# Performance work log

Measured on AMD Instinct MI355X. Metric: run time of the kernel, lower is better.

Reference implementation:

```python
import jax, jax.numpy as jnp
import numpy as np

LAMBDA = 0.7
RATIO = 3
EPS = 1e-6


def setup_inputs() -> dict:
    key = jax.random.key(0)
    k1, k2, k3 = jax.random.split(key, 3)
    bs, n, w, h = 8, 7, 640, 640
    preds = jax.random.normal(k1, (bs, n, w, h), dtype=jnp.float32)
    labels = jax.random.randint(k2, (bs, n, w, h), 0, 2, dtype=jnp.int32)
    training_mask = jax.random.randint(k3, (bs, w, h), 0, 2, dtype=jnp.int32)
    return {"preds": preds, "labels": labels, "training_mask": training_mask}


def _dice(S, G):
    # S, G: [C, P]; per-channel dice coefficient, then mean over channels
    num = 2.0 * jnp.sum(S * G, axis=-1)
    den = jnp.sum(S * S, axis=-1) + jnp.sum(G * G, axis=-1) + EPS
    return jnp.mean(num / den)


def _single_sample(pred, label, mask):
    # pred, label: [n, P]; mask: [P]
    P = pred.shape[-1]
    p = jax.nn.sigmoid(pred)
    pred_n = p[-1] * mask            # masked full-text prediction
    label_n = label[-1] * mask

    # --- OHEM mask M (cal_M): keep all positives + top (ratio*n_pos) hardest negatives ---
    pos = pred_n >= 0.5
    n_pos = jnp.sum(pos)
    n_neg_all = jnp.sum(~pos)
    k = n_pos * RATIO
    # sigmoid outputs are in (0,1); sentinel -1 pushes positives to the end of the descending sort
    neg_vals = jnp.where(pos, -1.0, pred_n)
    sorted_desc = -jnp.sort(-neg_vals)
    thr = sorted_desc[jnp.clip(k - 1, 0, P - 1)]  # k-th largest negative score
    ohem_active = (n_neg_all > k) & (k > 0)
    M = jnp.where(ohem_active, (pred_n >= thr).astype(jnp.float32), 1.0)

    # L_c: dice loss on OHEM-selected full-text map
    L_c = 1.0 - _dice((pred_n * M)[None, :], (label_n * M)[None, :])

    # L_s: dice loss on shrunk kernels, gated by predicted text region W
    W = (pred_n >= 0.5).astype(jnp.float32)
    L_s = 1.0 - _dice(p[:-1] * W, label[:-1] * W)

    loss = LAMBDA * L_c + (1.0 - LAMBDA) * L_s
    return L_c, L_s, loss


def reference(preds, labels, training_mask):
    bs, n, w, h = preds.shape
    preds = preds.reshape(bs, n, w * h)
    labels = labels.reshape(bs, n, w * h).astype(jnp.float32)
    mask = training_mask.reshape(bs, w * h).astype(jnp.float32)
    L_c, L_s, loss = jax.vmap(_single_sample)(preds, labels, mask)
    # reduction='mean'
    return L_c.mean(), L_s.mean(), loss.mean()
```

## Files before the change

kernel.cpp:

```cpp
#include <hip/hip_runtime.h>

#define BS   8
#define NCH  7
#define PX   409600
#define NBIN 65536
#define NCHK 256
#define EPSF 1e-6f
#define NT   256
#define GXM  50
#define UM   4
#define ITM  2

__device__ __forceinline__ float sigf(float x) {
    return 1.0f / (1.0f + __expf(-x));
}

__device__ __forceinline__ unsigned wred_u(unsigned v) {
    #pragma unroll
    for (int o = 32; o; o >>= 1) v += __shfl_down(v, o);
    return v;
}

__device__ __forceinline__ void wred3_f(float& v0, float& v1, float& v2) {
    #pragma unroll
    for (int o = 32; o; o >>= 1) {
        float t0 = __shfl_down(v0, o);
        float t1 = __shfl_down(v1, o);
        float t2 = __shfl_down(v2, o);
        v0 += t0; v1 += t1; v2 += t2;
    }
}

__device__ void select2(const unsigned* __restrict__ chunks,
                        const unsigned* __restrict__ bins,
                        unsigned k, unsigned* out_bin, unsigned* out_rank) {
    __shared__ unsigned cs[256];
    int t = threadIdx.x;
    cs[t] = chunks[t];
    __syncthreads();
    #pragma unroll
    for (int off = 1; off < 256; off <<= 1) {
        unsigned v = cs[t];
        unsigned a = (t + off < 256) ? cs[t + off] : 0u;
        __syncthreads();
        cs[t] = v + a;
        __syncthreads();
    }
    {
        unsigned sfx  = cs[t];
        unsigned sfx1 = (t < 255) ? cs[t + 1] : 0u;
        if (sfx >= k && sfx1 < k) { *out_bin = (unsigned)t; *out_rank = k - sfx1; }
    }
    __syncthreads();
    unsigned chunk = *out_bin, krem = *out_rank;
    cs[t] = bins[chunk * 256 + t];
    __syncthreads();
    #pragma unroll
    for (int off = 1; off < 256; off <<= 1) {
        unsigned v = cs[t];
        unsigned a = (t + off < 256) ? cs[t + off] : 0u;
        __syncthreads();
        cs[t] = v + a;
        __syncthreads();
    }
    {
        unsigned sfx  = cs[t];
        unsigned sfx1 = (t < 255) ? cs[t + 1] : 0u;
        if (sfx >= krem && sfx1 < krem) {
            *out_bin  = chunk * 256 + (unsigned)t;
            *out_rank = krem - sfx1;
        }
    }
    __syncthreads();
}

__global__ __launch_bounds__(256) void k_main(
        const float* __restrict__ preds, const int* __restrict__ labels,
        const int* __restrict__ mask,
        float* __restrict__ psumA,
        unsigned* __restrict__ ppos,
        unsigned* __restrict__ pzero,
        float* __restrict__ psumB,
        unsigned* __restrict__ done) {
    const int tid = threadIdx.x;
    const int y = blockIdx.y;
    const int b = y / 6, c = y % 6;
    const int cb = blockIdx.x;
    const bool c0 = (c == 0);
    if (y == 0 && cb == 0 && tid == 0) *done = 0u;

    const float* pc = preds + ((size_t)b * NCH + c) * PX;
    const int*   lc = labels + ((size_t)b * NCH + c) * PX;
    const float* p6 = preds + ((size_t)b * NCH + 6) * PX;
    const int*   l6 = labels + ((size_t)b * NCH + 6) * PX;
    const int*   mk = mask + (size_t)b * PX;

    float sn = 0.f, sp = 0.f;
    unsigned slc = 0;
    float a0 = 0.f, a1 = 0.f;
    unsigned a2c = 0, cnt = 0;

    for (int it = 0; it < ITM; ++it) {
        const int gbase = cb * (NT * UM * ITM) + it * (NT * UM) + tid;
        float4 P6[UM]; int4 M[UM]; float4 P[UM]; int4 L[UM]; int4 L6[UM];
        #pragma unroll
        for (int q = 0; q < UM; q++) {
            int px = (gbase + q * NT) * 4;
            P6[q] = *(const float4*)(p6 + px);
            M[q]  = *(const int4*)(mk + px);
        }
        #pragma unroll
        for (int q = 0; q < UM; q++) {
            int px = (gbase + q * NT) * 4;
            P[q] = *(const float4*)(pc + px);
            L[q] = *(const int4*)(lc + px);
        }
        if (c0) {
            #pragma unroll
            for (int q = 0; q < UM; q++) {
                int px = (gbase + q * NT) * 4;
                L6[q] = *(const int4*)(l6 + px);
            }
        }
        __builtin_amdgcn_sched_barrier(0);

        #pragma unroll
        for (int q = 0; q < UM; q++) {
            float mm[4]  = {(float)M[q].x, (float)M[q].y, (float)M[q].z, (float)M[q].w};
            float p6a[4] = {P6[q].x, P6[q].y, P6[q].z, P6[q].w};
            float pa[4]  = {P[q].x, P[q].y, P[q].z, P[q].w};
            int   la[4]  = {L[q].x, L[q].y, L[q].z, L[q].w};
            int   l6a[4] = {L6[q].x, L6[q].y, L6[q].z, L6[q].w};
            #pragma unroll
            for (int v = 0; v < 4; v++) {
                float pn = sigf(p6a[v]) * mm[v];
                bool W   = (pn >= 0.5f);
                float s  = sigf(pa[v]);
                bool lw  = W && (la[v] != 0);
                sn += lw ? s : 0.0f;
                sp += W ? s * s : 0.0f;
                slc += lw ? 1u : 0u;
                if (c0) {
                    cnt += W ? 1u : (__float_as_uint(pn) == 0u ? 0x10000u : 0u);
                    bool ln = (l6a[v] != 0) && (mm[v] != 0.0f);
                    a0 += ln ? pn : 0.0f;
                    a1 += pn * pn;
                    a2c += ln ? 1u : 0u;
                }
            }
        }
    }

    __shared__ float red[4][3];
    __shared__ float redA[4][3];
    __shared__ unsigned redC[4];
    const int lane = tid & 63, wid = tid >> 6;
    float v0 = sn, v1 = sp, v2 = (float)slc;
    wred3_f(v0, v1, v2);
    if (lane == 0) { red[wid][0] = v0; red[wid][1] = v1; red[wid][2] = v2; }
    if (c0) {
        float u0 = a0, u1 = a1, u2 = (float)a2c;
        wred3_f(u0, u1, u2);
        unsigned cr = wred_u(cnt);
        if (lane == 0) { redA[wid][0] = u0; redA[wid][1] = u1; redA[wid][2] = u2; redC[wid] = cr; }
    }
    __syncthreads();
    if (tid < 3) {
        float tot = red[0][tid] + red[1][tid] + red[2][tid] + red[3][tid];
        psumB[((size_t)y * 3 + tid) * GXM + cb] = tot;
    }
    if (c0) {
        if (tid < 3) {
            float tot = redA[0][tid] + redA[1][tid] + redA[2][tid] + redA[3][tid];
            psumA[((size_t)b * 3 + tid) * GXM + cb] = tot;
        }
        if (tid == 3) {
            unsigned ct = redC[0] + redC[1] + redC[2] + redC[3];
            ppos[b * GXM + cb]  = ct & 0xFFFFu;
            pzero[b * GXM + cb] = ct >> 16;
        }
    }
}

__global__ __launch_bounds__(256) void k_sel(
        const float* __restrict__ preds, const int* __restrict__ labels,
        const int* __restrict__ mask,
        const float* __restrict__ psumA, const float* __restrict__ psumB,
        const unsigned* __restrict__ ppos, const unsigned* __restrict__ pzero,
        unsigned* __restrict__ histws, unsigned* __restrict__ chunkws,
        float* __restrict__ lcls, unsigned* __restrict__ done,
        float* __restrict__ out) {
    const int tid = threadIdx.x;
    const int b = blockIdx.x;
    const int lane = tid & 63, wid = tid >> 6;

    __shared__ float S[21];
    __shared__ unsigned C[2];
    if (tid < 21) S[tid] = 0.f;
    if (tid < 2) C[tid] = 0u;
    __syncthreads();
    {
        unsigned pc = 0, zc = 0;
        for (int i = tid; i < GXM; i += NT) {
            pc += ppos[b * GXM + i];
            zc += pzero[b * GXM + i];
        }
        pc = wred_u(pc); zc = wred_u(zc);
        if (lane == 0) { atomicAdd(&C[0], pc); atomicAdd(&C[1], zc); }
    }
    for (int i = tid; i < 3 * GXM; i += NT)
        atomicAdd(&S[18 + i / GXM], psumA[(size_t)b * 3 * GXM + i]);
    for (int i = tid; i < 6 * 3 * GXM; i += NT) {
        int cch = i / (3 * GXM);
        int j   = (i / GXM) % 3;
        atomicAdd(&S[j * 6 + cch], psumB[(size_t)b * 6 * 3 * GXM + i]);
    }
    __syncthreads();
    const unsigned np = C[0], zc = C[1];

    const unsigned k = np * 3u;
    const bool active = ((unsigned)PX - np > k) && (k > 0u);
    const unsigned nzneg = (unsigned)PX - np - zc;

    float Lc_b;
    if (!active || k >= nzneg) {
        Lc_b = 1.0f - 2.0f * S[18] / (S[19] + S[20] + EPSF);
    } else {
        unsigned* h1 = histws + (size_t)b * NBIN;
        unsigned* c1 = chunkws + (size_t)b * NCHK;
        const float* pr6 = preds + ((size_t)b * NCH + 6) * PX;
        const int*   lb6 = labels + ((size_t)b * NCH + 6) * PX;
        const int*   mk  = mask + (size_t)b * PX;

        for (int j = tid; j < NBIN; j += NT) h1[j] = 0u;
        for (int j = tid; j < NCHK; j += NT) c1[j] = 0u;
        __syncthreads();
        for (int gg = tid; gg < PX; gg += NT) {
            float pnx = sigf(pr6[gg]) * (float)mk[gg];
            if (pnx < 0.5f) {
                unsigned bits = __float_as_uint(pnx);
                if (bits) {
                    atomicAdd(&h1[bits >> 16], 1u);
                    atomicAdd(&c1[bits >> 24], 1u);
                }
            }
        }
        __syncthreads();
        if (tid == 0) { atomicAdd(&h1[0], zc); atomicAdd(&c1[0], zc); }
        __syncthreads();

        __shared__ unsigned rb, rr, rb2, rr2;
        select2(c1, h1, k, &rb, &rr);
        float thrv;
        if (rb == 0u) {
            thrv = 0.0f;
        } else {
            unsigned hi = rb;
            for (int j = tid; j < NBIN; j += NT) h1[j] = 0u;
            for (int j = tid; j < NCHK; j += NT) c1[j] = 0u;
            __syncthreads();
            for (int gg = tid; gg < PX; gg += NT) {
                float pnx = sigf(pr6[gg]) * (float)mk[gg];
                if (pnx < 0.5f) {
                    unsigned bits = __float_as_uint(pnx);
                    if (bits && (bits >> 16) == hi) {
                        unsigned lo = bits & 0xFFFFu;
                        atomicAdd(&h1[lo], 1u);
                        atomicAdd(&c1[lo >> 8], 1u);
                    }
                }
            }
            __syncthreads();
            select2(c1, h1, rr, &rb2, &rr2);
            thrv = __uint_as_float((hi << 16) | rb2);
        }
        float a0 = 0.f, a1 = 0.f, a2 = 0.f;
        for (int gg = tid; gg < PX; gg += NT) {
            float m   = (float)mk[gg];
            float pnx = sigf(pr6[gg]) * m;
            if (pnx >= thrv) {
                float ln = (float)lb6[gg] * m;
                a0 += pnx * ln;
                a1 += pnx * pnx;
                a2 += ln;
            }
        }
        __shared__ float aR[4][3];
        wred3_f(a0, a1, a2);
        if (lane == 0) { aR[wid][0] = a0; aR[wid][1] = a1; aR[wid][2] = a2; }
        __syncthreads();
        float A0 = aR[0][0] + aR[1][0] + aR[2][0] + aR[3][0];
        float A1 = aR[0][1] + aR[1][1] + aR[2][1] + aR[3][1];
        float A2 = aR[0][2] + aR[1][2] + aR[2][2] + aR[3][2];
        Lc_b = 1.0f - 2.0f * A0 / (A1 + A2 + EPSF);
    }

    float ls_acc = 0.f;
    #pragma unroll
    for (int c = 0; c < 6; c++)
        ls_acc += (2.0f * S[c]) / (S[6 + c] + S[12 + c] + EPSF);
    float Ls_b = 1.0f - ls_acc * (1.0f / 6.0f);

    if (tid == 0) {
        lcls[b * 2]     = Lc_b;
        lcls[b * 2 + 1] = Ls_b;
    }

    __shared__ unsigned tick;
    if (tid == 0) {
        __threadfence();
        tick = atomicAdd(done, 1u);
    }
    __syncthreads();
    if (tick != (unsigned)(BS - 1)) return;
    __threadfence();

    float Lc = 0.f, Ls = 0.f;
    if (tid < BS) { Lc = lcls[tid * 2]; Ls = lcls[tid * 2 + 1]; }
    #pragma unroll
    for (int o = 4; o; o >>= 1) { Lc += __shfl_down(Lc, o); Ls += __shfl_down(Ls, o); }
    if (tid == 0) {
        float lc_m = Lc * (1.0f / (float)BS);
        float ls_m = Ls * (1.0f / (float)BS);
        out[0] = lc_m;
        out[1] = ls_m;
        out[2] = 0.7f * lc_m + 0.3f * ls_m;
    }
}

extern "C" void kernel_launch(void* const* d_in, const int* in_sizes, int n_in,
                              void* d_out, int out_size, void* d_ws, size_t ws_size,
                              hipStream_t stream) {
    const float* preds = (const float*)d_in[0];
    const int* labels  = (const int*)d_in[1];
    const int* mask    = (const int*)d_in[2];
    float* out = (float*)d_out;

    float*    psumA   = (float*)d_ws;
    unsigned* ppos    = (unsigned*)(psumA + (size_t)BS * 3 * GXM);
    unsigned* pzero   = ppos + BS * GXM;
    float*    psumB   = (float*)(pzero + BS * GXM);
    unsigned* done    = (unsigned*)(psumB + (size_t)BS * 18 * GXM);
    float*    lcls    = (float*)(done + 8);
    unsigned* histws  = (unsigned*)(lcls + BS * 2);
    unsigned* chunkws = histws + (size_t)BS * NBIN;

    hipLaunchKernelGGL(k_main, dim3(GXM, BS * 6), dim3(NT), 0, stream,
                       preds, labels, mask, psumA, ppos, pzero, psumB, done);

    hipLaunchKernelGGL(k_sel, dim3(BS), dim3(NT), 0, stream,
                       preds, labels, mask, psumA, psumB, ppos, pzero,
                       histws, chunkws, lcls, done, out);
}
```

Before: 216.5 us.

## Process three kernel channels per block to reuse channel-6 and mask loads

Each k_main block now handles three shrunk-kernel channels instead of one, loading the full-text prediction and mask once per pixel and reusing them for all three channels. The grid shrinks from 48 to 16 rows per column, and ITM is raised so each block still covers the same pixel range. This cuts redundant reads of channel 6 and the mask and their sigmoid recomputation. In exchange there are fewer blocks in flight (800 vs 2400), which may lower memory-level parallelism.

```diff
diff --git a/kernel.cpp b/kernel.cpp
--- a/kernel.cpp
+++ b/kernel.cpp
@@ -8,8 +8,7 @@
 #define EPSF 1e-6f
 #define NT   256
 #define GXM  50
-#define UM   4
-#define ITM  2
+#define ITM  8
 
 __device__ __forceinline__ float sigf(float x) {
     return 1.0f / (1.0f + __expf(-x));
@@ -84,97 +83,96 @@
         unsigned* __restrict__ done) {
     const int tid = threadIdx.x;
     const int y = blockIdx.y;
-    const int b = y / 6, c = y % 6;
+    const int b = y >> 1, half = y & 1;
+    const int cbase = half * 3;
     const int cb = blockIdx.x;
-    const bool c0 = (c == 0);
+    const bool h0 = (half == 0);
     if (y == 0 && cb == 0 && tid == 0) *done = 0u;
 
-    const float* pc = preds + ((size_t)b * NCH + c) * PX;
-    const int*   lc = labels + ((size_t)b * NCH + c) * PX;
-    const float* p6 = preds + ((size_t)b * NCH + 6) * PX;
-    const int*   l6 = labels + ((size_t)b * NCH + 6) * PX;
-    const int*   mk = mask + (size_t)b * PX;
-
-    float sn = 0.f, sp = 0.f;
-    unsigned slc = 0;
+    const float* p6  = preds + ((size_t)b * NCH + 6) * PX;
+    const int*   l6  = labels + ((size_t)b * NCH + 6) * PX;
+    const int*   mk  = mask + (size_t)b * PX;
+    const float* pc0 = preds + ((size_t)b * NCH + cbase) * PX;
+    const int*   lc0 = labels + ((size_t)b * NCH + cbase) * PX;
+
+    float sn[3] = {0.f, 0.f, 0.f}, sp[3] = {0.f, 0.f, 0.f};
+    unsigned sl[3] = {0u, 0u, 0u};
     float a0 = 0.f, a1 = 0.f;
     unsigned a2c = 0, cnt = 0;
 
     for (int it = 0; it < ITM; ++it) {
-        const int gbase = cb * (NT * UM * ITM) + it * (NT * UM) + tid;
-        float4 P6[UM]; int4 M[UM]; float4 P[UM]; int4 L[UM]; int4 L6[UM];
+        const int g  = cb * (NT * ITM) + it * NT + tid;
+        const int px = g * 4;
+        float4 P6 = *(const float4*)(p6 + px);
+        int4   M  = *(const int4*)(mk + px);
+        int4   L6 = make_int4(0, 0, 0, 0);
+        if (h0) L6 = *(const int4*)(l6 + px);
+        float4 P[3]; int4 L[3];
         #pragma unroll
-        for (int q = 0; q < UM; q++) {
-            int px = (gbase + q * NT) * 4;
-            P6[q] = *(const float4*)(p6 + px);
-            M[q]  = *(const int4*)(mk + px);
-        }
+        for (int c = 0; c < 3; c++) {
+            P[c] = *(const float4*)(pc0 + (size_t)c * PX + px);
+            L[c] = *(const int4*)(lc0 + (size_t)c * PX + px);
+        }
+        __builtin_amdgcn_sched_barrier(0);
+
+        float mm[4]  = {(float)M.x, (float)M.y, (float)M.z, (float)M.w};
+        float p6a[4] = {P6.x, P6.y, P6.z, P6.w};
+        int   l6a[4] = {L6.x, L6.y, L6.z, L6.w};
         #pragma unroll
-        for (int q = 0; q < UM; q++) {
-            int px = (gbase + q * NT) * 4;
-            P[q] = *(const float4*)(pc + px);
-            L[q] = *(const int4*)(lc + px);
-        }
-        if (c0) {
+        for (int v = 0; v < 4; v++) {
+            float pn = sigf(p6a[v]) * mm[v];
+            bool W   = (pn >= 0.5f);
+            if (h0) {
+                cnt += W ? 1u : (__float_as_uint(pn) == 0u ? 0x10000u : 0u);
+                bool ln = (l6a[v] != 0) && (mm[v] != 0.0f);
+                a0 += ln ? pn : 0.0f;
+                a1 += pn * pn;
+                a2c += ln ? 1u : 0u;
+            }
+            float pv[3] = {((const float*)&P[0])[v], ((const float*)&P[1])[v],
+                           ((const float*)&P[2])[v]};
+            int   lv[3] = {((const int*)&L[0])[v], ((const int*)&L[1])[v],
+                           ((const int*)&L[2])[v]};
             #pragma unroll
-            for (int q = 0; q < UM; q++) {
-                int px = (gbase + q * NT) * 4;
-                L6[q] = *(const int4*)(l6 + px);
-            }
-        }
-        __builtin_amdgcn_sched_barrier(0);
-
-        #pragma unroll
-        for (int q = 0; q < UM; q++) {
-            float mm[4]  = {(float)M[q].x, (float)M[q].y, (float)M[q].z, (float)M[q].w};
-            float p6a[4] = {P6[q].x, P6[q].y, P6[q].z, P6[q].w};
-            float pa[4]  = {P[q].x, P[q].y, P[q].z, P[q].w};
-            int   la[4]  = {L[q].x, L[q].y, L[q].z, L[q].w};
-            int   l6a[4] = {L6[q].x, L6[q].y, L6[q].z, L6[q].w};
-            #pragma unroll
-            for (int v = 0; v < 4; v++) {
-                float pn = sigf(p6a[v]) * mm[v];
-                bool W   = (pn >= 0.5f);
-                float s  = sigf(pa[v]);
-                bool lw  = W && (la[v] != 0);
-                sn += lw ? s : 0.0f;
-                sp += W ? s * s : 0.0f;
-                slc += lw ? 1u : 0u;
-                if (c0) {
-                    cnt += W ? 1u : (__float_as_uint(pn) == 0u ? 0x10000u : 0u);
-                    bool ln = (l6a[v] != 0) && (mm[v] != 0.0f);
-                    a0 += ln ? pn : 0.0f;
-                    a1 += pn * pn;
-                    a2c += ln ? 1u : 0u;
-                }
-            }
-        }
-    }
-
-    __shared__ float red[4][3];
+            for (int c = 0; c < 3; c++) {
+                float s = sigf(pv[c]);
+                bool lw = W && (lv[c] != 0);
+                sn[c] += lw ? s : 0.0f;
+                sp[c] += W ? s * s : 0.0f;
+                sl[c] += lw ? 1u : 0u;
+            }
+        }
+    }
+
+    __shared__ float red[4][3][3];
     __shared__ float redA[4][3];
     __shared__ unsigned redC[4];
     const int lane = tid & 63, wid = tid >> 6;
-    float v0 = sn, v1 = sp, v2 = (float)slc;
-    wred3_f(v0, v1, v2);
-    if (lane == 0) { red[wid][0] = v0; red[wid][1] = v1; red[wid][2] = v2; }
-    if (c0) {
+    #pragma unroll
+    for (int c = 0; c < 3; c++) {
+        float v0 = sn[c], v1 = sp[c], v2 = (float)sl[c];
+        wred3_f(v0, v1, v2);
+        if (lane == 0) { red[wid][c][0] = v0; red[wid][c][1] = v1; red[wid][c][2] = v2; }
+    }
+    if (h0) {
         float u0 = a0, u1 = a1, u2 = (float)a2c;
         wred3_f(u0, u1, u2);
         unsigned cr = wred_u(cnt);
         if (lane == 0) { redA[wid][0] = u0; redA[wid][1] = u1; redA[wid][2] = u2; redC[wid] = cr; }
     }
     __syncthreads();
-    if (tid < 3) {
-        float tot = red[0][tid] + red[1][tid] + red[2][tid] + red[3][tid];
-        psumB[((size_t)y * 3 + tid) * GXM + cb] = tot;
-    }
-    if (c0) {
-        if (tid < 3) {
-            float tot = redA[0][tid] + redA[1][tid] + redA[2][tid] + redA[3][tid];
-            psumA[((size_t)b * 3 + tid) * GXM + cb] = tot;
-        }
-        if (tid == 3) {
+    if (tid < 9) {
+        int c = tid / 3, j = tid % 3;
+        float tot = red[0][c][j] + red[1][c][j] + red[2][c][j] + red[3][c][j];
+        psumB[((size_t)(b * 6 + cbase + c) * 3 + j) * GXM + cb] = tot;
+    }
+    if (h0) {
+        if (tid >= 9 && tid < 12) {
+            int j = tid - 9;
+            float tot = redA[0][j] + redA[1][j] + redA[2][j] + redA[3][j];
+            psumA[((size_t)b * 3 + j) * GXM + cb] = tot;
+        }
+        if (tid == 12) {
             unsigned ct = redC[0] + redC[1] + redC[2] + redC[3];
             ppos[b * GXM + cb]  = ct & 0xFFFFu;
             pzero[b * GXM + cb] = ct >> 16;
@@ -345,7 +343,7 @@
     unsigned* histws  = (unsigned*)(lcls + BS * 2);
     unsigned* chunkws = histws + (size_t)BS * NBIN;
 
-    hipLaunchKernelGGL(k_main, dim3(GXM, BS * 6), dim3(NT), 0, stream,
+    hipLaunchKernelGGL(k_main, dim3(GXM, BS * 2), dim3(NT), 0, stream,
                        preds, labels, mask, psumA, ppos, pzero, psumB, done);
 
     hipLaunchKernelGGL(k_sel, dim3(BS), dim3(NT), 0, stream,
```

New measurement: 219.9 us. About the same (+1.5%).
